# Optimization experiments

Measured on AMD Instinct MI355X. Metric: run time of the kernel, lower is better.

Reference implementation:

```python
import jax, jax.numpy as jnp
import numpy as np

N = 100000      # nodes
E = 1600000     # edges (before self-loops)
F_IN = 128      # dataset.num_node_features
H, C = 8, 8     # heads, hid
D = H * C       # 64, concat output dim
G = 64          # graphs in batch
N_CLS = 10
SLOPE = 0.2     # PyG GATConv negative_slope default


def setup_inputs() -> dict:
    key = jax.random.key(0)
    ks = jax.random.split(key, 16)
    s = 0.1
    return {
        "x": jax.random.normal(ks[0], (N, F_IN), jnp.float32),
        "edge_index": jax.random.randint(ks[1], (2, E), 0, N, jnp.int32),
        "batch": jnp.sort(jax.random.randint(ks[2], (N,), 0, G, jnp.int32)),
        "W1": jax.random.normal(ks[3], (F_IN, D), jnp.float32) * s,
        "a1_src": jax.random.normal(ks[4], (H, C), jnp.float32) * s,
        "a1_dst": jax.random.normal(ks[5], (H, C), jnp.float32) * s,
        "b1": jnp.zeros((D,), jnp.float32),
        "W2": jax.random.normal(ks[6], (D, D), jnp.float32) * s,
        "a2_src": jax.random.normal(ks[7], (H, C), jnp.float32) * s,
        "a2_dst": jax.random.normal(ks[8], (H, C), jnp.float32) * s,
        "b2": jnp.zeros((D,), jnp.float32),
        "W3": jax.random.normal(ks[9], (D, D), jnp.float32) * s,
        "a3_src": jax.random.normal(ks[10], (H, C), jnp.float32) * s,
        "a3_dst": jax.random.normal(ks[11], (H, C), jnp.float32) * s,
        "b3": jnp.zeros((D,), jnp.float32),
        "lin_W": jax.random.normal(ks[12], (D, N_CLS), jnp.float32) * s,
        "lin_b": jnp.zeros((N_CLS,), jnp.float32),
    }


def _gat_conv(h_in, src, dst, W, a_src, a_dst, b):
    # h: [N, H, C] per-head projected features
    h = (h_in @ W).reshape(N, H, C)
    al_src = jnp.einsum('nhc,hc->nh', h, a_src)  # [N, H]
    al_dst = jnp.einsum('nhc,hc->nh', h, a_dst)
    e = al_src[src] + al_dst[dst]                # [E', H]
    e = jnp.where(e > 0, e, SLOPE * e)           # LeakyReLU
    # segment softmax over incoming edges of each dst node
    m = jax.ops.segment_max(e, dst, num_segments=N)          # every node has a self-loop
    e = jnp.exp(e - m[dst])
    denom = jax.ops.segment_sum(e, dst, num_segments=N)
    alpha = e / denom[dst]                        # [E', H]
    out = jax.ops.segment_sum(h[src] * alpha[:, :, None], dst, num_segments=N)
    return out.reshape(N, D) + b


def reference(x, edge_index, batch, W1, a1_src, a1_dst, b1,
              W2, a2_src, a2_dst, b2, W3, a3_src, a3_dst, b3, lin_W, lin_b):
    # PyG GATConv add_self_loops=True
    loop = jnp.arange(N, dtype=edge_index.dtype)
    src = jnp.concatenate([edge_index[0], loop])
    dst = jnp.concatenate([edge_index[1], loop])

    h = jax.nn.elu(_gat_conv(x, src, dst, W1, a1_src, a1_dst, b1))
    h = jax.nn.elu(_gat_conv(h, src, dst, W2, a2_src, a2_dst, b2))
    h = jax.nn.elu(_gat_conv(h, src, dst, W3, a3_src, a3_dst, b3))

    # global mean pool over graph assignment
    sums = jax.ops.segment_sum(h, batch, num_segments=G)          # [G, D]
    cnts = jax.ops.segment_sum(jnp.ones((N,), h.dtype), batch, num_segments=G)
    pooled = sums / jnp.maximum(cnts, 1.0)[:, None]

    return pooled @ lin_W + lin_b  # [G, N_CLS]
```

## Files before the change

### kernel.cpp

```cpp
#include <hip/hip_runtime.h>
#include <math.h>

#define NN 100000
#define EE 1600000
#define GG 64
#define NCLS 10

#define BSH 8
#define NB 391
#define EPH 8192
#define EPS 4096
#define CAPS 5120

typedef unsigned int uint32;

__device__ __forceinline__ unsigned short f2bf(float f) {
    unsigned u = __float_as_uint(f);
    unsigned r = (u + 0x7fffu + ((u >> 16) & 1u)) >> 16;
    return (unsigned short)r;
}


__global__ __launch_bounds__(512) void bhist_kernel(const int* __restrict__ dst,
                                                    int* __restrict__ bcnt, int n) {
    __shared__ int h[NB];
    int tid = threadIdx.x;
    for (int i = tid; i < NB; i += 512) h[i] = 0;
    __syncthreads();
    int e0 = blockIdx.x * EPH;
    int e1 = min(e0 + EPH, n);
    for (int e = e0 + tid; e < e1; e += 512) atomicAdd(&h[dst[e] >> BSH], 1);
    __syncthreads();
    for (int i = tid; i < NB; i += 512)
        if (h[i]) atomicAdd(&bcnt[i], h[i]);
}

__global__ __launch_bounds__(512) void bscan_kernel(const int* __restrict__ bcnt,
                                                    int* __restrict__ bbase) {
    __shared__ int s[512];
    int tid = threadIdx.x;
    int v = (tid < NB) ? bcnt[tid] : 0;
    s[tid] = v;
    __syncthreads();
    for (int off = 1; off < 512; off <<= 1) {
        int t = (tid >= off) ? s[tid - off] : 0;
        __syncthreads();
        s[tid] += t;
        __syncthreads();
    }
    if (tid < NB) bbase[tid + 1] = s[tid];
    if (tid == 0) bbase[0] = 0;
}

__global__ __launch_bounds__(512) void bscatter_kernel(
    const int* __restrict__ src, const int* __restrict__ dst,
    int* __restrict__ bfill, const int* __restrict__ bbase,
    uint32* __restrict__ bpack, int n) {
    __shared__ int hist[512], gbase[512], lbase[512], cnt2[512], sc[512];
    __shared__ uint32 lsd[EPS];
    __shared__ unsigned short bkt[EPS];
    int tid = threadIdx.x;
    int e0 = blockIdx.x * EPS;
    int e1 = min(e0 + EPS, n);

    hist[tid] = 0;
    cnt2[tid] = 0;
    __syncthreads();
    for (int e = e0 + tid; e < e1; e += 512) atomicAdd(&hist[dst[e] >> BSH], 1);
    __syncthreads();
    sc[tid] = hist[tid];
    __syncthreads();
    for (int off = 1; off < 512; off <<= 1) {
        int t = (tid >= off) ? sc[tid - off] : 0;
        __syncthreads();
        sc[tid] += t;
        __syncthreads();
    }
    lbase[tid] = sc[tid] - hist[tid];
    int go = hist[tid] > 0 ? atomicAdd(&bfill[tid], hist[tid]) : 0;
    gbase[tid] = ((tid < NB) ? bbase[tid] : 0) + go - lbase[tid];
    __syncthreads();
    for (int e = e0 + tid; e < e1; e += 512) {
        int s = src[e], dd = dst[e];
        int b = dd >> BSH;
        int r = atomicAdd(&cnt2[b], 1);
        int slot = lbase[b] + r;
        lsd[slot] = ((uint32)s << 8) | (uint32)(dd & 255);
        bkt[slot] = (unsigned short)b;
    }
    __syncthreads();
    int m = e1 - e0;
    for (int i = tid; i < m; i += 512)
        bpack[gbase[bkt[i]] + i] = lsd[i];
}

__global__ __launch_bounds__(256) void bsort_kernel(
    const uint32* __restrict__ bpack, const int* __restrict__ bbase,
    int* __restrict__ rowptr, int* __restrict__ col) {
    __shared__ int cnt[256], cnt2[256], sc[256];
    __shared__ int stage[CAPS];
    int b = blockIdx.x;
    int tid = threadIdx.x;
    int ebeg = bbase[b], eend = bbase[b + 1];
    int n0 = b << BSH;
    int nn = min(256, NN - n0);

    cnt[tid] = 0;
    cnt2[tid] = 0;
    __syncthreads();
    for (int e = ebeg + tid; e < eend; e += 256) atomicAdd(&cnt[bpack[e] & 255u], 1);
    __syncthreads();
    sc[tid] = cnt[tid];
    __syncthreads();
    for (int off = 1; off < 256; off <<= 1) {
        int t = (tid >= off) ? sc[tid - off] : 0;
        __syncthreads();
        sc[tid] += t;
        __syncthreads();
    }
    int excl = sc[tid] - cnt[tid];
    sc[tid] = excl;
    if (tid < nn) rowptr[n0 + tid] = ebeg + excl;
    if (b == NB - 1 && tid == 0) rowptr[NN] = eend;
    __syncthreads();
    int sz = eend - ebeg;
    bool fits = sz <= CAPS;
    for (int e = ebeg + tid; e < eend; e += 256) {
        uint32 p = bpack[e];
        int dl = (int)(p & 255u);
        int r = atomicAdd(&cnt2[dl], 1);
        int pos = sc[dl] + r;
        if (fits) stage[pos] = (int)(p >> 8);
        else col[ebeg + pos] = (int)(p >> 8);
    }
    __syncthreads();
    if (fits)
        for (int i = tid; i < sz; i += 256) col[ebeg + i] = stage[i];
}


template <int K>
__global__ __launch_bounds__(256) void gemm_al_kernel(
    const float* __restrict__ X, const float* __restrict__ W,
    const float* __restrict__ a_src, const float* __restrict__ a_dst,
    unsigned short* __restrict__ H, float* __restrict__ ALs, float* __restrict__ ALd,
    int nrows) {
    __shared__ float Xs[64 * K];
    __shared__ float Ws[K * 64];
    int tid = threadIdx.x;
    int r0 = blockIdx.x * 64;

    {
        const float4* Wg = (const float4*)W;
        float4* Ws4 = (float4*)Ws;
        for (int i = tid; i < K * 16; i += 256) Ws4[i] = Wg[i];
    }
    {
        const float4* Xg = (const float4*)(X + (size_t)r0 * K);
        float4* Xs4 = (float4*)Xs;
        const int nq = 64 * K / 4;
        int valid_q = (min(64, nrows - r0) * K) / 4;
        for (int i = tid; i < nq; i += 256)
            Xs4[i] = (i < valid_q) ? Xg[i] : make_float4(0.f, 0.f, 0.f, 0.f);
    }
    __syncthreads();

    int cg = tid & 15, rg = tid >> 4;
    int rbase = rg * 4;
    float4 acc0 = make_float4(0.f, 0.f, 0.f, 0.f);
    float4 acc1 = acc0, acc2 = acc0, acc3 = acc0;

#pragma unroll 2
    for (int k = 0; k < K; k += 4) {
        float4 x0 = *(const float4*)&Xs[(rbase + 0) * K + k];
        float4 x1 = *(const float4*)&Xs[(rbase + 1) * K + k];
        float4 x2 = *(const float4*)&Xs[(rbase + 2) * K + k];
        float4 x3 = *(const float4*)&Xs[(rbase + 3) * K + k];
        float4 w0 = *(const float4*)&Ws[(k + 0) * 64 + 4 * cg];
        float4 w1 = *(const float4*)&Ws[(k + 1) * 64 + 4 * cg];
        float4 w2 = *(const float4*)&Ws[(k + 2) * 64 + 4 * cg];
        float4 w3 = *(const float4*)&Ws[(k + 3) * 64 + 4 * cg];
#define FMA4(A, S, WV) \
        A.x = fmaf(S, WV.x, A.x); A.y = fmaf(S, WV.y, A.y); \
        A.z = fmaf(S, WV.z, A.z); A.w = fmaf(S, WV.w, A.w)
        FMA4(acc0, x0.x, w0); FMA4(acc1, x1.x, w0); FMA4(acc2, x2.x, w0); FMA4(acc3, x3.x, w0);
        FMA4(acc0, x0.y, w1); FMA4(acc1, x1.y, w1); FMA4(acc2, x2.y, w1); FMA4(acc3, x3.y, w1);
        FMA4(acc0, x0.z, w2); FMA4(acc1, x1.z, w2); FMA4(acc2, x2.z, w2); FMA4(acc3, x3.z, w2);
        FMA4(acc0, x0.w, w3); FMA4(acc1, x1.w, w3); FMA4(acc2, x2.w, w3); FMA4(acc3, x3.w, w3);
#undef FMA4
    }

    int hh = cg >> 1;
    float4 as4 = ((const float4*)a_src)[cg];
    float4 ad4 = ((const float4*)a_dst)[cg];
    float4 accs[4] = {acc0, acc1, acc2, acc3};
#pragma unroll
    for (int i = 0; i < 4; ++i) {
        int r = r0 + rbase + i;
        if (r < nrows) {
            ushort4 p;
            p.x = f2bf(accs[i].x); p.y = f2bf(accs[i].y);
            p.z = f2bf(accs[i].z); p.w = f2bf(accs[i].w);
            ((ushort4*)H)[(size_t)r * 16 + cg] = p;
            float ps = accs[i].x * as4.x + accs[i].y * as4.y +
                       accs[i].z * as4.z + accs[i].w * as4.w;
            float pd = accs[i].x * ad4.x + accs[i].y * ad4.y +
                       accs[i].z * ad4.z + accs[i].w * ad4.w;
            ps += __shfl_xor(ps, 1);
            pd += __shfl_xor(pd, 1);
            if ((cg & 1) == 0) {
                ALs[r * 8 + hh] = ps;
                ALd[r * 8 + hh] = pd;
            }
        }
    }
}


__global__ __launch_bounds__(256, 6) void agg_kernel(
    const unsigned short* __restrict__ H, const float* __restrict__ ALs,
    const float* __restrict__ ALd, const int* __restrict__ rowptr,
    const int* __restrict__ col, const float* __restrict__ bias,
    float* __restrict__ Out, int n) {
    int tid = threadIdx.x;
    int lane = tid & 63;
    int slot = lane >> 3, head = lane & 7;
    int wid = blockIdx.x * 4 + (tid >> 6);
    int d = wid * 8 + slot;
    bool active = d < n;
    if (!active) d = n - 1;
    const uint4* __restrict__ Hq = (const uint4*)H;

    float ad = ALd[d * 8 + head];
    float acc0 = 0.f, acc1 = 0.f, acc2 = 0.f, acc3 = 0.f;
    float acc4 = 0.f, acc5 = 0.f, acc6 = 0.f, acc7 = 0.f;
    float wsum = 0.f;

#define FMA8(U, W) { \
    acc0 = fmaf(W, __uint_as_float((U).x << 16), acc0); \
    acc1 = fmaf(W, __uint_as_float((U).x & 0xffff0000u), acc1); \
    acc2 = fmaf(W, __uint_as_float((U).y << 16), acc2); \
    acc3 = fmaf(W, __uint_as_float((U).y & 0xffff0000u), acc3); \
    acc4 = fmaf(W, __uint_as_float((U).z << 16), acc4); \
    acc5 = fmaf(W, __uint_as_float((U).z & 0xffff0000u), acc5); \
    acc6 = fmaf(W, __uint_as_float((U).w << 16), acc6); \
    acc7 = fmaf(W, __uint_as_float((U).w & 0xffff0000u), acc7); }

    {
        uint4 u = Hq[(size_t)d * 8 + head];
        float e = ALs[d * 8 + head] + ad;
        e = fmaxf(e, 0.2f * e);
        float w = __expf(e);
        FMA8(u, w);
        wsum = w;
    }

    int k = rowptr[d], re = rowptr[d + 1];
    for (; k + 4 <= re; k += 4) {
        int s0 = col[k], s1 = col[k + 1], s2 = col[k + 2], s3 = col[k + 3];
        uint4 u0 = Hq[(size_t)s0 * 8 + head];
        uint4 u1 = Hq[(size_t)s1 * 8 + head];
        uint4 u2 = Hq[(size_t)s2 * 8 + head];
        uint4 u3 = Hq[(size_t)s3 * 8 + head];
        float a0 = ALs[s0 * 8 + head];
        float a1 = ALs[s1 * 8 + head];
        float a2 = ALs[s2 * 8 + head];
        float a3 = ALs[s3 * 8 + head];
        float e0 = a0 + ad; e0 = fmaxf(e0, 0.2f * e0); float w0 = __expf(e0);
        float e1 = a1 + ad; e1 = fmaxf(e1, 0.2f * e1); float w1 = __expf(e1);
        float e2 = a2 + ad; e2 = fmaxf(e2, 0.2f * e2); float w2 = __expf(e2);
        float e3 = a3 + ad; e3 = fmaxf(e3, 0.2f * e3); float w3 = __expf(e3);
        FMA8(u0, w0);
        FMA8(u1, w1);
        FMA8(u2, w2);
        FMA8(u3, w3);
        wsum += (w0 + w1) + (w2 + w3);
    }
    if (k + 2 <= re) {
        int s0 = col[k], s1 = col[k + 1];
        uint4 u0 = Hq[(size_t)s0 * 8 + head];
        uint4 u1 = Hq[(size_t)s1 * 8 + head];
        float a0 = ALs[s0 * 8 + head];
        float a1 = ALs[s1 * 8 + head];
        float e0 = a0 + ad; e0 = fmaxf(e0, 0.2f * e0); float w0 = __expf(e0);
        float e1 = a1 + ad; e1 = fmaxf(e1, 0.2f * e1); float w1 = __expf(e1);
        FMA8(u0, w0);
        FMA8(u1, w1);
        wsum += w0 + w1;
        k += 2;
    }
    if (k < re) {
        int s = col[k];
        uint4 u = Hq[(size_t)s * 8 + head];
        float a = ALs[s * 8 + head];
        float e = a + ad; e = fmaxf(e, 0.2f * e);
        float w = __expf(e);
        FMA8(u, w);
        wsum += w;
    }
#undef FMA8

    if (active) {
        float inv = 1.f / wsum;
        float4 b0 = ((const float4*)bias)[head * 2];
        float4 b1 = ((const float4*)bias)[head * 2 + 1];
        float4 o0, o1;
        o0.x = fmaf(acc0, inv, b0.x); o0.x = o0.x > 0.f ? o0.x : expm1f(o0.x);
        o0.y = fmaf(acc1, inv, b0.y); o0.y = o0.y > 0.f ? o0.y : expm1f(o0.y);
        o0.z = fmaf(acc2, inv, b0.z); o0.z = o0.z > 0.f ? o0.z : expm1f(o0.z);
        o0.w = fmaf(acc3, inv, b0.w); o0.w = o0.w > 0.f ? o0.w : expm1f(o0.w);
        o1.x = fmaf(acc4, inv, b1.x); o1.x = o1.x > 0.f ? o1.x : expm1f(o1.x);
        o1.y = fmaf(acc5, inv, b1.y); o1.y = o1.y > 0.f ? o1.y : expm1f(o1.y);
        o1.z = fmaf(acc6, inv, b1.z); o1.z = o1.z > 0.f ? o1.z : expm1f(o1.z);
        o1.w = fmaf(acc7, inv, b1.w); o1.w = o1.w > 0.f ? o1.w : expm1f(o1.w);
        ((float4*)Out)[(size_t)d * 16 + head * 2] = o0;
        ((float4*)Out)[(size_t)d * 16 + head * 2 + 1] = o1;
    }
}


__global__ void pool_kernel(const float* __restrict__ H, const int* __restrict__ batch,
                            float* __restrict__ sums, float* __restrict__ cnt, int n) {
    int gw = (int)((blockIdx.x * blockDim.x + threadIdx.x) >> 6);
    int lane = threadIdx.x & 63;
    int n0 = gw * 64;
    if (n0 >= n) return;
    int n1 = min(n0 + 64, n);
    int curb = batch[n0];
    float local = 0.f, c_local = 0.f;
    for (int i = n0; i < n1; ++i) {
        int b = batch[i];
        if (b != curb) {
            atomicAdd(&sums[curb * 64 + lane], local);
            if (lane == 0) atomicAdd(&cnt[curb], c_local);
            local = 0.f;
            c_local = 0.f;
            curb = b;
        }
        local += H[(size_t)i * 64 + lane];
        c_local += 1.f;
    }
    atomicAdd(&sums[curb * 64 + lane], local);
    if (lane == 0) atomicAdd(&cnt[curb], c_local);
}

__global__ void final_kernel(const float* __restrict__ sums, const float* __restrict__ cnt,
                             const float* __restrict__ W, const float* __restrict__ b,
                             float* __restrict__ out) {
    int t = blockIdx.x * blockDim.x + threadIdx.x;
    if (t >= GG * NCLS) return;
    int g = t / NCLS, k = t % NCLS;
    float c = cnt[g];
    if (c < 1.f) c = 1.f;
    float inv = 1.f / c;
    float acc = b[k];
#pragma unroll
    for (int cc = 0; cc < 64; ++cc)
        acc = fmaf(sums[g * 64 + cc] * inv, W[cc * NCLS + k], acc);
    out[t] = acc;
}


extern "C" void kernel_launch(void* const* d_in, const int* in_sizes, int n_in,
                              void* d_out, int out_size, void* d_ws, size_t ws_size,
                              hipStream_t stream) {
    const float* x    = (const float*)d_in[0];
    const int*   ei   = (const int*)d_in[1];
    const int*   batch = (const int*)d_in[2];
    const float* W1 = (const float*)d_in[3];
    const float* a1s = (const float*)d_in[4];
    const float* a1d = (const float*)d_in[5];
    const float* b1 = (const float*)d_in[6];
    const float* W2 = (const float*)d_in[7];
    const float* a2s = (const float*)d_in[8];
    const float* a2d = (const float*)d_in[9];
    const float* b2 = (const float*)d_in[10];
    const float* W3 = (const float*)d_in[11];
    const float* a3s = (const float*)d_in[12];
    const float* a3d = (const float*)d_in[13];
    const float* b3 = (const float*)d_in[14];
    const float* linW = (const float*)d_in[15];
    const float* linb = (const float*)d_in[16];
    float* out = (float*)d_out;

    char* ws = (char*)d_ws;
    size_t off = 0;
    auto alloc = [&](size_t bytes) -> void* {
        void* p = ws + off;
        off = (off + bytes + 255) & ~(size_t)255;
        return p;
    };
    unsigned short* hBf = (unsigned short*)alloc((size_t)NN * 64 * 2);
    float* hF     = (float*)alloc((size_t)NN * 64 * 4);
    float* ALs    = (float*)alloc((size_t)NN * 8 * 4);
    float* ALd    = (float*)alloc((size_t)NN * 8 * 4);
    int*   rowptr = (int*)alloc((size_t)(NN + 1) * 4);
    int*   bcnt   = (int*)alloc(NB * 4);
    int*   bfill  = (int*)alloc(NB * 4);
    int*   bbase  = (int*)alloc((NB + 1) * 4);
    uint32* bpack = (uint32*)alloc((size_t)EE * 4);
    int*   col    = (int*)alloc((size_t)EE * 4);
    float* sums   = (float*)alloc((size_t)(GG * 64 + GG) * 4);
    float* gcnt   = sums + GG * 64;

    const int NBLK = (NN + 255) / 256;
    const int HB = (EE + EPH - 1) / EPH;
    const int SB = (EE + EPS - 1) / EPS;

    hipMemsetAsync(bcnt, 0, NB * 4, stream);
    hipMemsetAsync(bfill, 0, NB * 4, stream);
    bhist_kernel<<<HB, 512, 0, stream>>>(ei + EE, bcnt, EE);
    bscan_kernel<<<1, 512, 0, stream>>>(bcnt, bbase);
    bscatter_kernel<<<SB, 512, 0, stream>>>(ei, ei + EE, bfill, bbase, bpack, EE);
    bsort_kernel<<<NB, 256, 0, stream>>>(bpack, bbase, rowptr, col);

    const int GB = (NN + 63) / 64;
    const int AB = (NN + 31) / 32;

    gemm_al_kernel<128><<<GB, 256, 0, stream>>>(x, W1, a1s, a1d, hBf, ALs, ALd, NN);
    agg_kernel<<<AB, 256, 0, stream>>>(hBf, ALs, ALd, rowptr, col, b1, hF, NN);

    gemm_al_kernel<64><<<GB, 256, 0, stream>>>(hF, W2, a2s, a2d, hBf, ALs, ALd, NN);
    agg_kernel<<<AB, 256, 0, stream>>>(hBf, ALs, ALd, rowptr, col, b2, hF, NN);

    gemm_al_kernel<64><<<GB, 256, 0, stream>>>(hF, W3, a3s, a3d, hBf, ALs, ALd, NN);
    agg_kernel<<<AB, 256, 0, stream>>>(hBf, ALs, ALd, rowptr, col, b3, hF, NN);

    hipMemsetAsync(sums, 0, (size_t)(GG * 64 + GG) * 4, stream);
    pool_kernel<<<NBLK, 256, 0, stream>>>(hF, batch, sums, gcnt, NN);
    final_kernel<<<3, 256, 0, stream>>>(sums, gcnt, linW, linb, out);
}
```

Baseline: 429.1 us.

## Use wave-shuffle scans, padded buckets for vector loads, and padded GEMM LDS rows

Replaces the shared-memory Hillis-Steele scans in the bucket scan, scatter and sort kernels with wave-level shuffle scans followed by a small cross-wave step, cutting barrier count. Bucket bases are rounded up to multiples of four so bsort can read bpack and write col with 16-byte vector accesses. Since rows are no longer contiguous, CSR now keeps separate row-start and row-end arrays. The GEMM's X tile in LDS is padded by four floats per row to reduce bank conflicts. The two counter memsets are merged into one. The cost is an extra rowend array and padded edge buffers.

```diff
diff --git a/kernel.cpp b/kernel.cpp
--- a/kernel.cpp
+++ b/kernel.cpp
@@ -37,18 +37,30 @@
 
 __global__ __launch_bounds__(512) void bscan_kernel(const int* __restrict__ bcnt,
                                                     int* __restrict__ bbase) {
-    __shared__ int s[512];
     int tid = threadIdx.x;
-    int v = (tid < NB) ? bcnt[tid] : 0;
-    s[tid] = v;
-    __syncthreads();
-    for (int off = 1; off < 512; off <<= 1) {
-        int t = (tid >= off) ? s[tid - off] : 0;
-        __syncthreads();
-        s[tid] += t;
-        __syncthreads();
-    }
-    if (tid < NB) bbase[tid + 1] = s[tid];
+    int lane = tid & 63, wv = tid >> 6;
+    int v = (tid < NB) ? ((bcnt[tid] + 3) & ~3) : 0;
+    int inc = v;
+#pragma unroll
+    for (int off = 1; off < 64; off <<= 1) {
+        int t = __shfl_up(inc, off);
+        if (lane >= off) inc += t;
+    }
+    __shared__ int wtot[8];
+    if (lane == 63) wtot[wv] = inc;
+    __syncthreads();
+    if (tid < 8) {
+        int t = wtot[tid];
+#pragma unroll
+        for (int off = 1; off < 8; off <<= 1) {
+            int u = __shfl_up(t, off, 8);
+            if (tid >= off) t += u;
+        }
+        wtot[tid] = t;
+    }
+    __syncthreads();
+    if (wv > 0) inc += wtot[wv - 1];
+    if (tid < NB) bbase[tid + 1] = inc;
     if (tid == 0) bbase[0] = 0;
 }
 
@@ -56,10 +68,12 @@
     const int* __restrict__ src, const int* __restrict__ dst,
     int* __restrict__ bfill, const int* __restrict__ bbase,
     uint32* __restrict__ bpack, int n) {
-    __shared__ int hist[512], gbase[512], lbase[512], cnt2[512], sc[512];
+    __shared__ int hist[512], gbase[512], lbase[512], cnt2[512];
+    __shared__ int wtot[8];
     __shared__ uint32 lsd[EPS];
     __shared__ unsigned short bkt[EPS];
     int tid = threadIdx.x;
+    int lane = tid & 63, wv = tid >> 6;
     int e0 = blockIdx.x * EPS;
     int e1 = min(e0 + EPS, n);
 
@@ -68,17 +82,30 @@
     __syncthreads();
     for (int e = e0 + tid; e < e1; e += 512) atomicAdd(&hist[dst[e] >> BSH], 1);
     __syncthreads();
-    sc[tid] = hist[tid];
-    __syncthreads();
-    for (int off = 1; off < 512; off <<= 1) {
-        int t = (tid >= off) ? sc[tid - off] : 0;
-        __syncthreads();
-        sc[tid] += t;
-        __syncthreads();
-    }
-    lbase[tid] = sc[tid] - hist[tid];
-    int go = hist[tid] > 0 ? atomicAdd(&bfill[tid], hist[tid]) : 0;
-    gbase[tid] = ((tid < NB) ? bbase[tid] : 0) + go - lbase[tid];
+    int h = hist[tid];
+    int inc = h;
+#pragma unroll
+    for (int off = 1; off < 64; off <<= 1) {
+        int t = __shfl_up(inc, off);
+        if (lane >= off) inc += t;
+    }
+    if (lane == 63) wtot[wv] = inc;
+    __syncthreads();
+    if (tid < 8) {
+        int t = wtot[tid];
+#pragma unroll
+        for (int off = 1; off < 8; off <<= 1) {
+            int u = __shfl_up(t, off, 8);
+            if (tid >= off) t += u;
+        }
+        wtot[tid] = t;
+    }
+    __syncthreads();
+    if (wv > 0) inc += wtot[wv - 1];
+    int lb = inc - h;
+    lbase[tid] = lb;
+    int go = h > 0 ? atomicAdd(&bfill[tid], h) : 0;
+    gbase[tid] = ((tid < NB) ? bbase[tid] : 0) + go - lb;
     __syncthreads();
     for (int e = e0 + tid; e < e1; e += 512) {
         int s = src[e], dd = dst[e];
@@ -96,46 +123,92 @@
 
 __global__ __launch_bounds__(256) void bsort_kernel(
     const uint32* __restrict__ bpack, const int* __restrict__ bbase,
-    int* __restrict__ rowptr, int* __restrict__ col) {
-    __shared__ int cnt[256], cnt2[256], sc[256];
+    const int* __restrict__ bcnt,
+    int* __restrict__ rp, int* __restrict__ re, int* __restrict__ col) {
+    __shared__ int cnt[256], cnt2[256];
+    __shared__ int wtot[4];
     __shared__ int stage[CAPS];
     int b = blockIdx.x;
     int tid = threadIdx.x;
-    int ebeg = bbase[b], eend = bbase[b + 1];
+    int lane = tid & 63, wv = tid >> 6;
+    int ebeg = bbase[b];
+    int sz = bcnt[b];
     int n0 = b << BSH;
     int nn = min(256, NN - n0);
 
     cnt[tid] = 0;
     cnt2[tid] = 0;
     __syncthreads();
-    for (int e = ebeg + tid; e < eend; e += 256) atomicAdd(&cnt[bpack[e] & 255u], 1);
-    __syncthreads();
-    sc[tid] = cnt[tid];
-    __syncthreads();
-    for (int off = 1; off < 256; off <<= 1) {
-        int t = (tid >= off) ? sc[tid - off] : 0;
-        __syncthreads();
-        sc[tid] += t;
-        __syncthreads();
-    }
-    int excl = sc[tid] - cnt[tid];
-    sc[tid] = excl;
-    if (tid < nn) rowptr[n0 + tid] = ebeg + excl;
-    if (b == NB - 1 && tid == 0) rowptr[NN] = eend;
-    __syncthreads();
-    int sz = eend - ebeg;
+    const uint4* bq = (const uint4*)(bpack + ebeg);
+    int nq = sz >> 2;
+    for (int i = tid; i < nq; i += 256) {
+        uint4 p = bq[i];
+        atomicAdd(&cnt[p.x & 255u], 1);
+        atomicAdd(&cnt[p.y & 255u], 1);
+        atomicAdd(&cnt[p.z & 255u], 1);
+        atomicAdd(&cnt[p.w & 255u], 1);
+    }
+    for (int e = (nq << 2) + tid; e < sz; e += 256)
+        atomicAdd(&cnt[bpack[ebeg + e] & 255u], 1);
+    __syncthreads();
+    int c = cnt[tid];
+    int inc = c;
+#pragma unroll
+    for (int off = 1; off < 64; off <<= 1) {
+        int t = __shfl_up(inc, off);
+        if (lane >= off) inc += t;
+    }
+    if (lane == 63) wtot[wv] = inc;
+    __syncthreads();
+    if (tid < 4) {
+        int t = wtot[tid];
+#pragma unroll
+        for (int off = 1; off < 4; off <<= 1) {
+            int u = __shfl_up(t, off, 4);
+            if (tid >= off) t += u;
+        }
+        wtot[tid] = t;
+    }
+    __syncthreads();
+    if (wv > 0) inc += wtot[wv - 1];
+    int excl = inc - c;
+    cnt[tid] = excl;
+    if (tid < nn) {
+        rp[n0 + tid] = ebeg + excl;
+        re[n0 + tid] = ebeg + inc;
+    }
+    __syncthreads();
     bool fits = sz <= CAPS;
-    for (int e = ebeg + tid; e < eend; e += 256) {
-        uint32 p = bpack[e];
+    for (int i = tid; i < nq; i += 256) {
+        uint4 p = bq[i];
+        int d0 = (int)(p.x & 255u), d1 = (int)(p.y & 255u);
+        int d2 = (int)(p.z & 255u), d3 = (int)(p.w & 255u);
+        int p0 = cnt[d0] + atomicAdd(&cnt2[d0], 1);
+        int p1 = cnt[d1] + atomicAdd(&cnt2[d1], 1);
+        int p2 = cnt[d2] + atomicAdd(&cnt2[d2], 1);
+        int p3 = cnt[d3] + atomicAdd(&cnt2[d3], 1);
+        if (fits) {
+            stage[p0] = (int)(p.x >> 8); stage[p1] = (int)(p.y >> 8);
+            stage[p2] = (int)(p.z >> 8); stage[p3] = (int)(p.w >> 8);
+        } else {
+            col[ebeg + p0] = (int)(p.x >> 8); col[ebeg + p1] = (int)(p.y >> 8);
+            col[ebeg + p2] = (int)(p.z >> 8); col[ebeg + p3] = (int)(p.w >> 8);
+        }
+    }
+    for (int e = (nq << 2) + tid; e < sz; e += 256) {
+        uint32 p = bpack[ebeg + e];
         int dl = (int)(p & 255u);
-        int r = atomicAdd(&cnt2[dl], 1);
-        int pos = sc[dl] + r;
+        int pos = cnt[dl] + atomicAdd(&cnt2[dl], 1);
         if (fits) stage[pos] = (int)(p >> 8);
         else col[ebeg + pos] = (int)(p >> 8);
     }
     __syncthreads();
-    if (fits)
-        for (int i = tid; i < sz; i += 256) col[ebeg + i] = stage[i];
+    if (fits) {
+        uint4* colq = (uint4*)(col + ebeg);
+        const uint4* stq = (const uint4*)stage;
+        for (int i = tid; i < nq; i += 256) colq[i] = stq[i];
+        for (int i = (nq << 2) + tid; i < sz; i += 256) col[ebeg + i] = stage[i];
+    }
 }
 
 
@@ -145,7 +218,8 @@
     const float* __restrict__ a_src, const float* __restrict__ a_dst,
     unsigned short* __restrict__ H, float* __restrict__ ALs, float* __restrict__ ALd,
     int nrows) {
-    __shared__ float Xs[64 * K];
+    const int KP = K + 4;
+    __shared__ float Xs[64 * (K + 4)];
     __shared__ float Ws[K * 64];
     int tid = threadIdx.x;
     int r0 = blockIdx.x * 64;
@@ -157,11 +231,14 @@
     }
     {
         const float4* Xg = (const float4*)(X + (size_t)r0 * K);
-        float4* Xs4 = (float4*)Xs;
         const int nq = 64 * K / 4;
         int valid_q = (min(64, nrows - r0) * K) / 4;
-        for (int i = tid; i < nq; i += 256)
-            Xs4[i] = (i < valid_q) ? Xg[i] : make_float4(0.f, 0.f, 0.f, 0.f);
+        const int QPR = K / 4;
+        for (int i = tid; i < nq; i += 256) {
+            int row = i / QPR, wq = i % QPR;
+            float4 v = (i < valid_q) ? Xg[i] : make_float4(0.f, 0.f, 0.f, 0.f);
+            *(float4*)&Xs[row * KP + wq * 4] = v;
+        }
     }
     __syncthreads();
 
@@ -172,10 +249,10 @@
 
 #pragma unroll 2
     for (int k = 0; k < K; k += 4) {
-        float4 x0 = *(const float4*)&Xs[(rbase + 0) * K + k];
-        float4 x1 = *(const float4*)&Xs[(rbase + 1) * K + k];
-        float4 x2 = *(const float4*)&Xs[(rbase + 2) * K + k];
-        float4 x3 = *(const float4*)&Xs[(rbase + 3) * K + k];
+        float4 x0 = *(const float4*)&Xs[(rbase + 0) * KP + k];
+        float4 x1 = *(const float4*)&Xs[(rbase + 1) * KP + k];
+        float4 x2 = *(const float4*)&Xs[(rbase + 2) * KP + k];
+        float4 x3 = *(const float4*)&Xs[(rbase + 3) * KP + k];
         float4 w0 = *(const float4*)&Ws[(k + 0) * 64 + 4 * cg];
         float4 w1 = *(const float4*)&Ws[(k + 1) * 64 + 4 * cg];
         float4 w2 = *(const float4*)&Ws[(k + 2) * 64 + 4 * cg];
@@ -219,9 +296,9 @@
 
 __global__ __launch_bounds__(256, 6) void agg_kernel(
     const unsigned short* __restrict__ H, const float* __restrict__ ALs,
-    const float* __restrict__ ALd, const int* __restrict__ rowptr,
-    const int* __restrict__ col, const float* __restrict__ bias,
-    float* __restrict__ Out, int n) {
+    const float* __restrict__ ALd, const int* __restrict__ rp,
+    const int* __restrict__ re, const int* __restrict__ col,
+    const float* __restrict__ bias, float* __restrict__ Out, int n) {
     int tid = threadIdx.x;
     int lane = tid & 63;
     int slot = lane >> 3, head = lane & 7;
@@ -255,8 +332,8 @@
         wsum = w;
     }
 
-    int k = rowptr[d], re = rowptr[d + 1];
-    for (; k + 4 <= re; k += 4) {
+    int k = rp[d], kend = re[d];
+    for (; k + 4 <= kend; k += 4) {
         int s0 = col[k], s1 = col[k + 1], s2 = col[k + 2], s3 = col[k + 3];
         uint4 u0 = Hq[(size_t)s0 * 8 + head];
         uint4 u1 = Hq[(size_t)s1 * 8 + head];
@@ -276,7 +353,7 @@
         FMA8(u3, w3);
         wsum += (w0 + w1) + (w2 + w3);
     }
-    if (k + 2 <= re) {
+    if (k + 2 <= kend) {
         int s0 = col[k], s1 = col[k + 1];
         uint4 u0 = Hq[(size_t)s0 * 8 + head];
         uint4 u1 = Hq[(size_t)s1 * 8 + head];
@@ -289,7 +366,7 @@
         wsum += w0 + w1;
         k += 2;
     }
-    if (k < re) {
+    if (k < kend) {
         int s = col[k];
         uint4 u = Hq[(size_t)s * 8 + head];
         float a = ALs[s * 8 + head];
@@ -394,12 +471,13 @@
     float* hF     = (float*)alloc((size_t)NN * 64 * 4);
     float* ALs    = (float*)alloc((size_t)NN * 8 * 4);
     float* ALd    = (float*)alloc((size_t)NN * 8 * 4);
-    int*   rowptr = (int*)alloc((size_t)(NN + 1) * 4);
-    int*   bcnt   = (int*)alloc(NB * 4);
-    int*   bfill  = (int*)alloc(NB * 4);
+    int*   rp     = (int*)alloc((size_t)NN * 4);
+    int*   reArr  = (int*)alloc((size_t)NN * 4);
+    int*   bcnt   = (int*)alloc((size_t)2 * NB * 4);
+    int*   bfill  = bcnt + NB;
     int*   bbase  = (int*)alloc((NB + 1) * 4);
-    uint32* bpack = (uint32*)alloc((size_t)EE * 4);
-    int*   col    = (int*)alloc((size_t)EE * 4);
+    uint32* bpack = (uint32*)alloc(((size_t)EE + 4 * NB) * 4);
+    int*   col    = (int*)alloc(((size_t)EE + 4 * NB) * 4);
     float* sums   = (float*)alloc((size_t)(GG * 64 + GG) * 4);
     float* gcnt   = sums + GG * 64;
 
@@ -407,24 +485,23 @@
     const int HB = (EE + EPH - 1) / EPH;
     const int SB = (EE + EPS - 1) / EPS;
 
-    hipMemsetAsync(bcnt, 0, NB * 4, stream);
-    hipMemsetAsync(bfill, 0, NB * 4, stream);
+    hipMemsetAsync(bcnt, 0, (size_t)2 * NB * 4, stream);
     bhist_kernel<<<HB, 512, 0, stream>>>(ei + EE, bcnt, EE);
     bscan_kernel<<<1, 512, 0, stream>>>(bcnt, bbase);
     bscatter_kernel<<<SB, 512, 0, stream>>>(ei, ei + EE, bfill, bbase, bpack, EE);
-    bsort_kernel<<<NB, 256, 0, stream>>>(bpack, bbase, rowptr, col);
+    bsort_kernel<<<NB, 256, 0, stream>>>(bpack, bbase, bcnt, rp, reArr, col);
 
     const int GB = (NN + 63) / 64;
     const int AB = (NN + 31) / 32;
 
     gemm_al_kernel<128><<<GB, 256, 0, stream>>>(x, W1, a1s, a1d, hBf, ALs, ALd, NN);
-    agg_kernel<<<AB, 256, 0, stream>>>(hBf, ALs, ALd, rowptr, col, b1, hF, NN);
+    agg_kernel<<<AB, 256, 0, stream>>>(hBf, ALs, ALd, rp, reArr, col, b1, hF, NN);
 
     gemm_al_kernel<64><<<GB, 256, 0, stream>>>(hF, W2, a2s, a2d, hBf, ALs, ALd, NN);
-    agg_kernel<<<AB, 256, 0, stream>>>(hBf, ALs, ALd, rowptr, col, b2, hF, NN);
+    agg_kernel<<<AB, 256, 0, stream>>>(hBf, ALs, ALd, rp, reArr, col, b2, hF, NN);
 
     gemm_al_kernel<64><<<GB, 256, 0, stream>>>(hF, W3, a3s, a3d, hBf, ALs, ALd, NN);
-    agg_kernel<<<AB, 256, 0, stream>>>(hBf, ALs, ALd, rowptr, col, b3, hF, NN);
+    agg_kernel<<<AB, 256, 0, stream>>>(hBf, ALs, ALd, rp, reArr, col, b3, hF, NN);
 
     hipMemsetAsync(sums, 0, (size_t)(GG * 64 + GG) * 4, stream);
     pool_kernel<<<NBLK, 256, 0, stream>>>(hF, batch, sums, gcnt, NN);
```

New measurement: 414.9 us. -3.3%, faster.
